# Kernel optimization log

Measured on AMD Instinct MI355X. Metric: run time of the kernel, lower is better.

Reference implementation:

```python
import jax, jax.numpy as jnp
import numpy as np

B, S, D = 8, 2048, 1024

def setup_inputs() -> dict:
    key = jax.random.key(0)
    kq, kk, kv = jax.random.split(key, 3)
    qm = jax.random.normal(kq, (B, S, D), dtype=jnp.float32)
    km = jax.random.normal(kk, (B, S, D), dtype=jnp.float32)
    vm = jax.random.normal(kv, (B, S, D), dtype=jnp.float32)
    return {"qm": qm, "km": km, "vm": vm}

def reference(qm, km, vm):
    # qkm = qm @ km^T / sqrt(d_k)   -> [B, S, S]
    scale = 1.0 / jnp.sqrt(jnp.asarray(qm.shape[-1], dtype=qm.dtype))
    qkm = jnp.einsum('bqd,bkd->bqk', qm, km) * scale
    # NOTE: faithful to source: softmax is applied AFTER the second matmul,
    # i.e. softmax((QK^T/sqrt(d)) @ V, axis=-1). masking=False (module default).
    out = jnp.einsum('bqk,bkd->bqd', qkm, vm)  # [B, S, D]
    return jax.nn.softmax(out, axis=-1)
```

## Files before the change

### kernel.cpp

```cpp
#include <hip/hip_runtime.h>
#include <hip/hip_bf16.h>
#include <stdint.h>

#define BATCH 8
#define SEQ   2048
#define DIM   1024

typedef unsigned short u16;
typedef __attribute__((ext_vector_type(8))) short short8;
typedef __attribute__((ext_vector_type(4))) float f32x4;
typedef __attribute__((ext_vector_type(4))) unsigned short us4;

__device__ __forceinline__ u16 f2bf(float x){
  union { float f; uint32_t u; } c; c.f = x;
  uint32_t u = c.u;
  uint32_t r = u + 0x7fffu + ((u >> 16) & 1u);
  return (u16)(r >> 16);
}
__device__ __forceinline__ float bf2f(u16 s){
  union { uint32_t u; float f; } c; c.u = ((uint32_t)s) << 16;
  return c.f;
}

__device__ __forceinline__ void gload16(const void* g, void* l){
  __builtin_amdgcn_global_load_lds(
      (const __attribute__((address_space(1))) void*)g,
      (__attribute__((address_space(3))) void*)l, 16, 0, 0);
}

__global__ __launch_bounds__(256) void k_split(const float* __restrict__ src,
                                               u16* __restrict__ dst, int nchunk){
  for (int i = blockIdx.x*blockDim.x + threadIdx.x; i < nchunk; i += gridDim.x*blockDim.x){
    int r = i >> 8;
    int c = (i & 255) << 2;
    f32x4 v = *(const f32x4*)(src + (size_t)r*DIM + c);
    us4 h, l;
    #pragma unroll
    for (int j = 0; j < 4; j++){
      u16 hh = f2bf(v[j]);
      h[j] = hh;
      l[j] = f2bf(v[j] - bf2f(hh));
    }
    u16* d = dst + (size_t)r*(2*DIM) + c;
    *(us4*)d         = h;
    *(us4*)(d + DIM) = l;
  }
}

__global__ __launch_bounds__(256) void k_convert_kv(const float* __restrict__ K,
                                                    const float* __restrict__ V,
                                                    u16* __restrict__ Kt,
                                                    u16* __restrict__ Vt){
  __shared__ float tile[64][65];
  int z = blockIdx.z;
  const float* Src = (z < 8 ? K : V);
  u16* Dst = (z < 8 ? Kt : Vt);
  int zb = z & 7;
  const float* Vb = Src + (size_t)zb * SEQ * DIM;
  u16* Vtb = Dst + (size_t)zb * DIM * (2*SEQ);
  int s0 = blockIdx.x * 64, d0 = blockIdx.y * 64;
  int t = threadIdx.x;
  int rs = t >> 4;
  int cd = (t & 15) * 4;
  #pragma unroll
  for (int i = 0; i < 4; i++){
    int s = rs + i*16;
    f32x4 v = *(const f32x4*)(Vb + (size_t)(s0 + s)*DIM + d0 + cd);
    tile[s][cd+0] = v[0]; tile[s][cd+1] = v[1];
    tile[s][cd+2] = v[2]; tile[s][cd+3] = v[3];
  }
  __syncthreads();
  int dl = t >> 4;
  int sl = (t & 15) * 4;
  #pragma unroll
  for (int i = 0; i < 4; i++){
    int d = dl + i*16;
    us4 h, l;
    #pragma unroll
    for (int j = 0; j < 4; j++){
      float x = tile[sl+j][d];
      u16 hh = f2bf(x);
      h[j] = hh;
      l[j] = f2bf(x - bf2f(hh));
    }
    size_t off = (size_t)(d0 + d) * (2*SEQ) + s0 + sl;
    *(us4*)(Vtb + off)       = h;
    *(us4*)(Vtb + off + SEQ) = l;
  }
}

template<int KROW, int SPLITK, int SPLITOUT, int NOUT, int TX, int TY>
__global__ __launch_bounds__(256,4) void k_gemmS(const u16* __restrict__ A,
                                                 const u16* __restrict__ B,
                                                 void* __restrict__ Cout,
                                                 size_t aStride, size_t bStride, size_t cStride){
  constexpr int LA = 2*KROW;
  constexpr int ITER = (SPLITK ? 1024 : KROW) / 32;
  __shared__ __align__(16) u16 lds[4][128*32];

  int xcd = blockIdx.x & 7;
  int idx = blockIdx.x >> 3;
  int nPerX = gridDim.x >> 3;
  int gid = xcd * nPerX + idx;
  constexpr int TPZ = TX*TY;
  int z  = gid / TPZ;
  int rm = gid % TPZ;
  int bx = rm % TX;
  int by = rm / TX;

  int zb = SPLITK ? (z & 7) : z;
  int kh = SPLITK ? (z >> 3) : 0;

  const u16* Ab = A + (size_t)zb * aStride + (size_t)kh * 1024;
  const u16* Bb = B + (size_t)zb * bStride + (size_t)kh * 1024;

  int t = threadIdx.x, lane = t & 63, w = t >> 6;
  int wm = (w & 1) * 64, wn = (w >> 1) * 64;
  int fr = lane & 15;

  int srow    = lane >> 2;
  int srcSlot = ((lane & 3) ^ ((lane >> 3) & 3)) * 8;

  const u16* aBase = Ab + ((size_t)bx*128) * LA + srcSlot;
  const u16* bBase = Bb + ((size_t)by*128) * LA + srcSlot;

  int rdSlot = (((lane >> 4) ^ ((fr >> 1) & 3))) * 8;

  f32x4 acc[4][4] = {};

  for (int ti = 0; ti < ITER; ti++){
    size_t kof = (size_t)ti * 32;
    #pragma unroll
    for (int o = 0; o < 2; o++){
      int c = w*2 + o;
      size_t ro = (size_t)(c*16 + srow) * LA + kof;
      const u16* ga = aBase + ro;
      const u16* gb = bBase + ro;
      int le = c * 512;
      gload16(ga,        &lds[0][le]);
      gload16(ga + KROW, &lds[1][le]);
      gload16(gb,        &lds[2][le]);
      gload16(gb + KROW, &lds[3][le]);
    }
    __syncthreads();

    short8 fah[4], fal[4], fbh[4], fbl[4];
    #pragma unroll
    for (int mi = 0; mi < 4; mi++){
      fah[mi] = *(const short8*)&lds[0][(wm + mi*16 + fr)*32 + rdSlot];
      fal[mi] = *(const short8*)&lds[1][(wm + mi*16 + fr)*32 + rdSlot];
      fbh[mi] = *(const short8*)&lds[2][(wn + mi*16 + fr)*32 + rdSlot];
      fbl[mi] = *(const short8*)&lds[3][(wn + mi*16 + fr)*32 + rdSlot];
    }
    #pragma unroll
    for (int mi = 0; mi < 4; mi++){
      #pragma unroll
      for (int ni = 0; ni < 4; ni++){
        acc[mi][ni] = __builtin_amdgcn_mfma_f32_16x16x32_bf16(fah[mi], fbh[ni], acc[mi][ni], 0,0,0);
        acc[mi][ni] = __builtin_amdgcn_mfma_f32_16x16x32_bf16(fah[mi], fbl[ni], acc[mi][ni], 0,0,0);
        acc[mi][ni] = __builtin_amdgcn_mfma_f32_16x16x32_bf16(fal[mi], fbh[ni], acc[mi][ni], 0,0,0);
      }
    }
    __syncthreads();
  }

  int cr = (lane >> 4) * 4, cc = lane & 15;
  if (SPLITOUT){
    u16* Cb = (u16*)Cout + (size_t)z * cStride;
    const float scale = 0.03125f;
    #pragma unroll
    for (int mi = 0; mi < 4; mi++){
      int gr = bx*128 + wm + mi*16 + cr;
      #pragma unroll
      for (int ni = 0; ni < 4; ni++){
        int gc = by*128 + wn + ni*16 + cc;
        #pragma unroll
        for (int rr = 0; rr < 4; rr++){
          float x = acc[mi][ni][rr] * scale;
          u16 h = f2bf(x);
          u16 l = f2bf(x - bf2f(h));
          size_t off = (size_t)(gr + rr) * (2*NOUT) + gc;
          Cb[off]        = h;
          Cb[off + NOUT] = l;
        }
      }
    }
  } else {
    float* Cb = (float*)Cout + (size_t)z * cStride;
    #pragma unroll
    for (int mi = 0; mi < 4; mi++){
      int gr = bx*128 + wm + mi*16 + cr;
      #pragma unroll
      for (int ni = 0; ni < 4; ni++){
        int gc = by*128 + wn + ni*16 + cc;
        #pragma unroll
        for (int rr = 0; rr < 4; rr++){
          Cb[(size_t)(gr + rr) * NOUT + gc] = acc[mi][ni][rr];
        }
      }
    }
  }
}

__global__ __launch_bounds__(256) void k_reduce_split(const float* __restrict__ P,
                                                      u16* __restrict__ Ws){
  int i = blockIdx.x*256 + threadIdx.x;
  int rg = i >> 8;
  int c  = (i & 255) * 4;
  f32x4 a = *(const f32x4*)(P + (size_t)rg*1024 + c);
  f32x4 b = *(const f32x4*)(P + ((size_t)rg + 8192)*1024 + c);
  us4 h, l;
  #pragma unroll
  for (int j = 0; j < 4; j++){
    float x = (a[j] + b[j]) * 0.03125f;
    u16 hh = f2bf(x);
    h[j] = hh;
    l[j] = f2bf(x - bf2f(hh));
  }
  int zb = rg >> 10, d = rg & 1023;
  u16* Wb = Ws + (size_t)zb * ((size_t)DIM * 2*DIM);
  *(us4*)(Wb + (size_t)d*2048 + c)        = h;
  *(us4*)(Wb + (size_t)d*2048 + 1024 + c) = l;
}

__global__ __launch_bounds__(256) void k_softmax(float* __restrict__ O){
  float* p = O + (size_t)blockIdx.x * DIM;
  int t = threadIdx.x;
  int lane = t & 63, wave = t >> 6;
  f32x4 v = *(f32x4*)(p + t*4);
  float m = fmaxf(fmaxf(v[0], v[1]), fmaxf(v[2], v[3]));
  #pragma unroll
  for (int o = 32; o > 0; o >>= 1) m = fmaxf(m, __shfl_xor(m, o));
  __shared__ float rmax[4], rsum[4];
  if (lane == 0) rmax[wave] = m;
  __syncthreads();
  m = fmaxf(fmaxf(rmax[0], rmax[1]), fmaxf(rmax[2], rmax[3]));
  float e0 = expf(v[0]-m), e1 = expf(v[1]-m), e2 = expf(v[2]-m), e3 = expf(v[3]-m);
  float s = e0 + e1 + e2 + e3;
  #pragma unroll
  for (int o = 32; o > 0; o >>= 1) s += __shfl_xor(s, o);
  if (lane == 0) rsum[wave] = s;
  __syncthreads();
  s = rsum[0] + rsum[1] + rsum[2] + rsum[3];
  float inv = 1.0f / s;
  f32x4 rv = { e0*inv, e1*inv, e2*inv, e3*inv };
  *(f32x4*)(p + t*4) = rv;
}

extern "C" void kernel_launch(void* const* d_in, const int* in_sizes, int n_in,
                              void* d_out, int out_size, void* d_ws, size_t ws_size,
                              hipStream_t stream){
  const float* Q = (const float*)d_in[0];
  const float* K = (const float*)d_in[1];
  const float* V = (const float*)d_in[2];
  float* Out = (float*)d_out;
  u16* w = (u16*)d_ws;

  const size_t QsB = (size_t)SEQ * (2*DIM);
  const size_t KtB = (size_t)DIM * (2*SEQ);
  const size_t VtB = KtB;
  const size_t WsB = (size_t)DIM * (2*DIM);

  dim3 blk(256);
  dim3 cgrid(SEQ/64, DIM/64, 16);

  const size_t base2 = 8 * (KtB + VtB + WsB) * sizeof(u16);
  const size_t needA = base2 + (size_t)16*1024*1024*sizeof(float);
  const size_t needB = base2;

  if (ws_size >= needA){
    u16* Kt = w;
    u16* Vt = Kt + 8*KtB;
    u16* Ws = Vt + 8*VtB;
    float* Part = (float*)(Ws + 8*WsB);
    u16* Qs = w;
    k_convert_kv<<<cgrid, blk, 0, stream>>>(K, V, Kt, Vt);
    k_gemmS<SEQ, 1, 0, DIM, 8, 8><<<dim3(1024), blk, 0, stream>>>(
        Vt, Kt, Part, VtB, KtB, (size_t)1024*1024);
    k_reduce_split<<<dim3(8192), blk, 0, stream>>>(Part, Ws);
    k_split<<<dim3(2048), blk, 0, stream>>>(Q, Qs, 8*SEQ*(DIM/4));
    k_gemmS<DIM, 0, 0, DIM, 16, 8><<<dim3(1024), blk, 0, stream>>>(
        Qs, Ws, Out, QsB, WsB, (size_t)SEQ*DIM);
  } else if (ws_size >= needB){
    u16* Kt = w;
    u16* Vt = Kt + 8*KtB;
    u16* Ws = Vt + 8*VtB;
    u16* Qs = w;
    k_convert_kv<<<cgrid, blk, 0, stream>>>(K, V, Kt, Vt);
    k_gemmS<SEQ, 0, 1, DIM, 8, 8><<<dim3(512), blk, 0, stream>>>(
        Vt, Kt, Ws, VtB, KtB, WsB);
    k_split<<<dim3(2048), blk, 0, stream>>>(Q, Qs, 8*SEQ*(DIM/4));
    k_gemmS<DIM, 0, 0, DIM, 16, 8><<<dim3(1024), blk, 0, stream>>>(
        Qs, Ws, Out, QsB, WsB, (size_t)SEQ*DIM);
  } else {
    u16* Qs = w;
    u16* Kt = Qs + QsB;
    u16* Vt = Kt + KtB;
    u16* Ws = Vt + VtB;
    for (int b = 0; b < BATCH; b++){
      const size_t inOff = (size_t)b * SEQ * DIM;
      k_split<<<dim3(1024), blk, 0, stream>>>(Q + inOff, Qs, SEQ*(DIM/4));
      k_convert_kv<<<dim3(SEQ/64, DIM/64, 1), blk, 0, stream>>>(K + inOff, K + inOff, Kt, Kt);
      k_convert_kv<<<dim3(SEQ/64, DIM/64, 1), blk, 0, stream>>>(V + inOff, V + inOff, Vt, Vt);
      k_gemmS<SEQ, 0, 1, DIM, 8, 8><<<dim3(64), blk, 0, stream>>>(
          Vt, Kt, Ws, VtB, KtB, WsB);
      k_gemmS<DIM, 0, 0, DIM, 16, 8><<<dim3(128), blk, 0, stream>>>(
          Qs, Ws, Out + inOff, QsB, WsB, (size_t)SEQ*DIM);
    }
  }
  k_softmax<<<dim3(BATCH*SEQ), blk, 0, stream>>>(Out);
}
```

Measured before the change: 313.7 us.

## Add 256x256-tile double-buffered 8-wave GEMM kernel with interleaved prefetch

Adds a new GEMM kernel using 512-thread blocks with 256x256 output tiles and double-buffered LDS. Global-to-LDS prefetch of the next K-step is interleaved with MFMA issue, using explicit waitcnt, barriers, sched_barrier and setprio. Both the split-K V^T K GEMM and the Q·W GEMM now use it in the main paths. The larger tile is meant to raise operand reuse and hide load latency. In exchange it uses one block per CU, more LDS and registers, and fewer blocks (256), which risks poorer occupancy and load balance.

```diff
diff --git a/kernel.cpp b/kernel.cpp
--- a/kernel.cpp
+++ b/kernel.cpp
@@ -89,14 +89,14 @@
   }
 }
 
-template<int KROW, int SPLITK, int SPLITOUT, int NOUT, int TX, int TY>
-__global__ __launch_bounds__(256,4) void k_gemmS(const u16* __restrict__ A,
-                                                 const u16* __restrict__ B,
-                                                 void* __restrict__ Cout,
-                                                 size_t aStride, size_t bStride, size_t cStride){
+template<int KROW, int SPLITK, int TX, int TY>
+__global__ __launch_bounds__(512,1) void k8n(const u16* __restrict__ A,
+                                             const u16* __restrict__ B,
+                                             float* __restrict__ C,
+                                             size_t aStride, size_t bStride, size_t cStride){
   constexpr int LA = 2*KROW;
-  constexpr int ITER = (SPLITK ? 1024 : KROW) / 32;
-  __shared__ __align__(16) u16 lds[4][128*32];
+  constexpr int NT = (SPLITK ? 1024 : KROW) / 32;
+  __shared__ __align__(16) u16 lds[2][4][256*32];
 
   int xcd = blockIdx.x & 7;
   int idx = blockIdx.x >> 3;
@@ -107,7 +107,156 @@
   int rm = gid % TPZ;
   int bx = rm % TX;
   int by = rm / TX;
-
+  int zb = SPLITK ? (z & 7) : z;
+  int kh = SPLITK ? (z >> 3) : 0;
+
+  const u16* Ab = A + (size_t)zb * aStride + (size_t)kh * 1024;
+  const u16* Bb = B + (size_t)zb * bStride + (size_t)kh * 1024;
+  float* Cb = C + (size_t)z * cStride;
+
+  int t0 = threadIdx.x, lane = t0 & 63, wv = t0 >> 6;
+  int wm = (wv >> 2) * 128, wn = (wv & 3) * 64;
+  int fr = lane & 15;
+  int rdSlot  = ((lane >> 4) ^ ((fr >> 1) & 3)) * 8;
+  int srcSlot = ((lane & 3) ^ ((lane >> 3) & 3)) * 8;
+
+  int jj = wv*16 + (lane >> 2);
+  int gA = (jj & 63) + (jj >> 6) * 128;
+  int gB = (jj & 31) + (jj >> 5) * 64;
+
+  const u16* aB = Ab + (size_t)bx*256*LA + srcSlot;
+  const u16* bB = Bb + (size_t)by*256*LA + srcSlot;
+  int ldst = wv*512;
+
+  f32x4 acc[8][4] = {};
+  short8 aH[4], aL[4], b0H[2], b0L[2], b1H[2], b1L[2];
+
+  #define STAGE_QA(buf, t32, p) {                                             \
+    size_t ko = (size_t)(t32)*32 + (size_t)(gA + (p)*64)*LA;                  \
+    gload16(aB + ko,        &lds[buf][0][(p)*4096 + ldst]);                   \
+    gload16(aB + ko + KROW, &lds[buf][1][(p)*4096 + ldst]); }
+  #define STAGE_QB(buf, t32, p) {                                             \
+    size_t ko = (size_t)(t32)*32 + (size_t)(gB + (p)*32)*LA;                  \
+    gload16(bB + ko,        &lds[buf][2][(p)*4096 + ldst]);                   \
+    gload16(bB + ko + KROW, &lds[buf][3][(p)*4096 + ldst]); }
+
+  #define LD_A(buf, h) { _Pragma("unroll") for (int q = 0; q < 4; q++){       \
+      int g = wm + ((h)*4+q)*16 + fr;                                         \
+      int ja = (g & 63) + ((g >> 7) & 1)*64 + ((g >> 6) & 1)*128;             \
+      aH[q] = *(const short8*)&lds[buf][0][ja*32 + rdSlot];                   \
+      aL[q] = *(const short8*)&lds[buf][1][ja*32 + rdSlot]; } }
+  #define LD_B(buf, gb, BH, BL) { _Pragma("unroll") for (int n = 0; n < 2; n++){ \
+      int g = wn + ((gb)*2+n)*16 + fr;                                        \
+      int jb = (g & 31) + ((g >> 6) & 3)*32 + ((g >> 5) & 1)*128;             \
+      BH[n] = *(const short8*)&lds[buf][2][jb*32 + rdSlot];                   \
+      BL[n] = *(const short8*)&lds[buf][3][jb*32 + rdSlot]; } }
+
+  #define MM8(h, BH, BL, nb) { _Pragma("unroll") for (int q = 0; q < 4; q++){ \
+      _Pragma("unroll") for (int n = 0; n < 2; n++){                          \
+        f32x4 c0 = acc[(h)*4+q][(nb)+n];                                      \
+        c0 = __builtin_amdgcn_mfma_f32_16x16x32_bf16(aH[q], BH[n], c0, 0,0,0);\
+        c0 = __builtin_amdgcn_mfma_f32_16x16x32_bf16(aH[q], BL[n], c0, 0,0,0);\
+        c0 = __builtin_amdgcn_mfma_f32_16x16x32_bf16(aL[q], BH[n], c0, 0,0,0);\
+        acc[(h)*4+q][(nb)+n] = c0; } } }
+
+  #define SB0() __builtin_amdgcn_sched_barrier(0)
+
+  STAGE_QA(0, 0, 0) STAGE_QB(0, 0, 0) STAGE_QB(0, 0, 1) STAGE_QA(0, 0, 1)
+
+  for (int t = 0; t < NT; t++){
+    int buf = t & 1, sb = buf ^ 1;
+    bool st = (t + 1 < NT);
+    asm volatile("s_waitcnt vmcnt(4)" ::: "memory");
+    SB0();
+    __builtin_amdgcn_s_barrier();
+    SB0();
+    LD_A(buf, 0)
+    LD_B(buf, 0, b0H, b0L)
+    if (st) STAGE_QA(sb, t+1, 0)
+    __builtin_amdgcn_s_setprio(1);
+    MM8(0, b0H, b0L, 0)
+    __builtin_amdgcn_s_setprio(0);
+    if (st){ asm volatile("s_waitcnt vmcnt(2)" ::: "memory"); }
+    else   { asm volatile("s_waitcnt vmcnt(0)" ::: "memory"); }
+    SB0();
+    __builtin_amdgcn_s_barrier();
+    SB0();
+    LD_B(buf, 1, b1H, b1L)
+    if (st) STAGE_QB(sb, t+1, 0)
+    __builtin_amdgcn_s_setprio(1);
+    MM8(0, b1H, b1L, 2)
+    __builtin_amdgcn_s_setprio(0);
+    LD_A(buf, 1)
+    if (st) STAGE_QB(sb, t+1, 1)
+    __builtin_amdgcn_s_setprio(1);
+    MM8(1, b1H, b1L, 2)
+    __builtin_amdgcn_s_setprio(0);
+    if (st) STAGE_QA(sb, t+1, 1)
+    __builtin_amdgcn_s_setprio(1);
+    MM8(1, b0H, b0L, 0)
+    __builtin_amdgcn_s_setprio(0);
+  }
+
+  #undef STAGE_QA
+  #undef STAGE_QB
+  #undef LD_A
+  #undef LD_B
+  #undef MM8
+  #undef SB0
+
+  int cr = (lane >> 4) * 4;
+  #pragma unroll
+  for (int mi = 0; mi < 8; mi++){
+    int gr = bx*256 + wm + mi*16 + cr;
+    #pragma unroll
+    for (int ni = 0; ni < 4; ni++){
+      int gc = by*256 + wn + ni*16 + fr;
+      #pragma unroll
+      for (int e = 0; e < 4; e++)
+        Cb[(size_t)(gr + e) * 1024 + gc] = acc[mi][ni][e];
+    }
+  }
+}
+
+__global__ __launch_bounds__(256) void k_reduce_split(const float* __restrict__ P,
+                                                      u16* __restrict__ Ws){
+  int i = blockIdx.x*256 + threadIdx.x;
+  int rg = i >> 8;
+  int c  = (i & 255) * 4;
+  f32x4 a = *(const f32x4*)(P + (size_t)rg*1024 + c);
+  f32x4 b = *(const f32x4*)(P + ((size_t)rg + 8192)*1024 + c);
+  us4 h, l;
+  #pragma unroll
+  for (int j = 0; j < 4; j++){
+    float x = (a[j] + b[j]) * 0.03125f;
+    u16 hh = f2bf(x);
+    h[j] = hh;
+    l[j] = f2bf(x - bf2f(hh));
+  }
+  int zb = rg >> 10, d = rg & 1023;
+  u16* Wb = Ws + (size_t)zb * ((size_t)DIM * 2*DIM);
+  *(us4*)(Wb + (size_t)d*2048 + c)        = h;
+  *(us4*)(Wb + (size_t)d*2048 + 1024 + c) = l;
+}
+
+template<int KROW, int SPLITK, int SPLITOUT, int NOUT, int TX, int TY>
+__global__ __launch_bounds__(256,4) void k_gemmS(const u16* __restrict__ A,
+                                                 const u16* __restrict__ B,
+                                                 void* __restrict__ Cout,
+                                                 size_t aStride, size_t bStride, size_t cStride){
+  constexpr int LA = 2*KROW;
+  constexpr int ITER = (SPLITK ? 1024 : KROW) / 32;
+  __shared__ __align__(16) u16 lds[4][128*32];
+
+  int xcd = blockIdx.x & 7;
+  int idx = blockIdx.x >> 3;
+  int nPerX = gridDim.x >> 3;
+  int gid = xcd * nPerX + idx;
+  constexpr int TPZ = TX*TY;
+  int z  = gid / TPZ;
+  int rm = gid % TPZ;
+  int bx = rm % TX;
+  int by = rm / TX;
   int zb = SPLITK ? (z & 7) : z;
   int kh = SPLITK ? (z >> 3) : 0;
 
@@ -117,13 +266,11 @@
   int t = threadIdx.x, lane = t & 63, w = t >> 6;
   int wm = (w & 1) * 64, wn = (w >> 1) * 64;
   int fr = lane & 15;
-
   int srow    = lane >> 2;
   int srcSlot = ((lane & 3) ^ ((lane >> 3) & 3)) * 8;
 
   const u16* aBase = Ab + ((size_t)bx*128) * LA + srcSlot;
   const u16* bBase = Bb + ((size_t)by*128) * LA + srcSlot;
-
   int rdSlot = (((lane >> 4) ^ ((fr >> 1) & 3))) * 8;
 
   f32x4 acc[4][4] = {};
@@ -202,27 +349,6 @@
   }
 }
 
-__global__ __launch_bounds__(256) void k_reduce_split(const float* __restrict__ P,
-                                                      u16* __restrict__ Ws){
-  int i = blockIdx.x*256 + threadIdx.x;
-  int rg = i >> 8;
-  int c  = (i & 255) * 4;
-  f32x4 a = *(const f32x4*)(P + (size_t)rg*1024 + c);
-  f32x4 b = *(const f32x4*)(P + ((size_t)rg + 8192)*1024 + c);
-  us4 h, l;
-  #pragma unroll
-  for (int j = 0; j < 4; j++){
-    float x = (a[j] + b[j]) * 0.03125f;
-    u16 hh = f2bf(x);
-    h[j] = hh;
-    l[j] = f2bf(x - bf2f(hh));
-  }
-  int zb = rg >> 10, d = rg & 1023;
-  u16* Wb = Ws + (size_t)zb * ((size_t)DIM * 2*DIM);
-  *(us4*)(Wb + (size_t)d*2048 + c)        = h;
-  *(us4*)(Wb + (size_t)d*2048 + 1024 + c) = l;
-}
-
 __global__ __launch_bounds__(256) void k_softmax(float* __restrict__ O){
   float* p = O + (size_t)blockIdx.x * DIM;
   int t = threadIdx.x;
@@ -275,11 +401,11 @@
     float* Part = (float*)(Ws + 8*WsB);
     u16* Qs = w;
     k_convert_kv<<<cgrid, blk, 0, stream>>>(K, V, Kt, Vt);
-    k_gemmS<SEQ, 1, 0, DIM, 8, 8><<<dim3(1024), blk, 0, stream>>>(
+    k8n<SEQ, 1, 4, 4><<<dim3(256), dim3(512), 0, stream>>>(
         Vt, Kt, Part, VtB, KtB, (size_t)1024*1024);
     k_reduce_split<<<dim3(8192), blk, 0, stream>>>(Part, Ws);
     k_split<<<dim3(2048), blk, 0, stream>>>(Q, Qs, 8*SEQ*(DIM/4));
-    k_gemmS<DIM, 0, 0, DIM, 16, 8><<<dim3(1024), blk, 0, stream>>>(
+    k8n<DIM, 0, 8, 4><<<dim3(256), dim3(512), 0, stream>>>(
         Qs, Ws, Out, QsB, WsB, (size_t)SEQ*DIM);
   } else if (ws_size >= needB){
     u16* Kt = w;
@@ -290,7 +416,7 @@
     k_gemmS<SEQ, 0, 1, DIM, 8, 8><<<dim3(512), blk, 0, stream>>>(
         Vt, Kt, Ws, VtB, KtB, WsB);
     k_split<<<dim3(2048), blk, 0, stream>>>(Q, Qs, 8*SEQ*(DIM/4));
-    k_gemmS<DIM, 0, 0, DIM, 16, 8><<<dim3(1024), blk, 0, stream>>>(
+    k8n<DIM, 0, 8, 4><<<dim3(256), dim3(512), 0, stream>>>(
         Qs, Ws, Out, QsB, WsB, (size_t)SEQ*DIM);
   } else {
     u16* Qs = w;
```

Measured after the change: 267.5 us. 14.7% less time.
